# Performance work log

Measured on AMD Instinct MI355X. Metric: run time of the kernel, lower is better.

## Reference

```python
import jax, jax.numpy as jnp
import numpy as np

ALPHA = 1.0
MIN_FEATURE_SIZE = 1.0
SC = 1e-12                      # stabilizer added to first derivatives
EPS_V_FLOOR = 1e-32 / 6.0       # torch.tensor(1e-32 ** 1 / 6) == 1e-32/6 (** binds tighter than /)


def _grad2d(phi, d):
    """Vectorized equivalent of numerical_gradient_2d: central differences in the
    interior, one-sided forward/backward differences at the boundaries."""
    gx = jnp.concatenate([
        (phi[1:2, :] - phi[0:1, :]) / d,           # forward diff at i == 0
        (phi[2:, :] - phi[:-2, :]) / (2.0 * d),    # central diff in interior
        (phi[-1:, :] - phi[-2:-1, :]) / d,         # backward diff at i == H-1
    ], axis=0)
    gy = jnp.concatenate([
        (phi[:, 1:2] - phi[:, 0:1]) / d,
        (phi[:, 2:] - phi[:, :-2]) / (2.0 * d),
        (phi[:, -1:] - phi[:, -2:-1]) / d,
    ], axis=1)
    return gx, gy


def setup_inputs() -> dict:
    key = jax.random.key(0)
    eps = jax.random.normal(key, (4096, 4096), dtype=jnp.float32)
    grid_size = jnp.asarray(0.05, dtype=jnp.float32)
    return {"eps": eps, "grid_size": grid_size}


def reference(eps, grid_size):
    # mirror the field along axis 1 (torch.cat((eps, eps.flip(1)), dim=1)) -> [H, 2W]
    eps = jnp.concatenate([eps, eps[:, ::-1]], axis=1)

    # ls_derivatives: first derivatives (+SC), then second derivatives of those
    eps_x, eps_y = _grad2d(eps, grid_size)
    eps_x = eps_x + SC
    eps_y = eps_y + SC
    eps_xx, eps_xy = _grad2d(eps_x, grid_size)
    _, eps_yy = _grad2d(eps_y, grid_size)

    pi_d = np.pi / (1.1 * MIN_FEATURE_SIZE)
    eps_v = jnp.maximum(jnp.sqrt(eps_x**2 + eps_y**2), EPS_V_FLOOR)
    k = (eps_x**2 * eps_yy - 2.0 * eps_x * eps_y * eps_xy + eps_y**2 * eps_xx) / eps_v**3
    curve_const = jnp.abs(k * jnp.arctan(eps_v / eps)) - pi_d
    return jnp.nansum(ALPHA * jnp.maximum(curve_const, 0.0) * grid_size**2)
```

## Files before the change

### kernel.cpp

```cpp
#include <hip/hip_runtime.h>
#include <math.h>


#define BLOCK_X 256
#define ROWS_PER 16

__device__ __forceinline__ float fast_atan_ratio(float v, float c, float rv)
{
    const float rc = __builtin_amdgcn_rcpf(c);
    const float q  = v * rc;
    const float iq = c * rv;
    const bool  big = fabsf(q) > 1.0f;
    const float t  = big ? iq : q;
    const float s  = t * t;
    float p = fmaf(s, -0.01172120f, 0.05265332f);
    p = fmaf(s, p, -0.11643287f);
    p = fmaf(s, p,  0.19354346f);
    p = fmaf(s, p, -0.33262347f);
    p = fmaf(s, p,  0.99997726f);
    const float at = p * t;
    const float hp = copysignf(1.57079632679f, q);
    return big ? (hp - at) : at;
}

__device__ __forceinline__ float interior_rows(
    const float* __restrict__ eps, int Wn, int i0, int j, float rd2)
{
    const float SC = 1e-12f;
    const float FLOORV = (float)(1e-32 / 6.0);
    const float pi_d = 3.14159265358979323846f / 1.1f;
    const float rd22 = rd2 * rd2;

    const float* p0 = eps + (size_t)(i0 - 2) * (size_t)Wn + j;
    const float* p1 = p0 + Wn;
    const float* p2 = p1 + Wn;
    const float* p3 = p2 + Wn;
    const float* p4 = p3 + Wn;

    float acc = 0.0f;
    #pragma unroll
    for (int r = 0; r < ROWS_PER; ++r) {
        const float e_nn = p0[0];
        const float e_nw = p1[-1], e_n = p1[0], e_ne = p1[1];
        const float e_ww = p2[-2], e_w = p2[-1], e_c = p2[0],
                    e_e  = p2[1],  e_ee = p2[2];
        const float e_sw = p3[-1], e_s = p3[0], e_se = p3[1];
        const float e_ss = p4[0];

        const float ex = fmaf(e_s - e_n, rd2, SC);
        const float ey = fmaf(e_e - e_w, rd2, SC);
        const float exx = fmaf(-2.0f, e_c, e_ss + e_nn) * rd22;
        const float eyy = fmaf(-2.0f, e_c, e_ee + e_ww) * rd22;
        const float exy = ((e_se - e_ne) - (e_sw - e_nw)) * rd22;

        const float t1 = ex * ex;
        const float t2 = ey * ey;
        const float exy2 = exy + exy;
        float num = t1 * eyy;
        num = fmaf(t2, exx, num);
        num = fmaf(-(ex * ey), exy2, num);

        float ev = __builtin_amdgcn_sqrtf(t1 + t2);
        ev = fmaxf(ev, FLOORV);
        const float rv = __builtin_amdgcn_rcpf(ev);
        const float k  = num * (rv * rv) * rv;
        const float at = fast_atan_ratio(ev, e_c, rv);
        const float cc = fabsf(k * at) - pi_d;
        acc += fmaxf(cc, 0.0f);

        p0 = p1; p1 = p2; p2 = p3; p3 = p4; p4 += Wn;
    }
    return acc;
}

__device__ float generic_rows(const float* __restrict__ eps, int Hn, int Wn,
                              int i0, int j, float rd)
{
    const float rd2 = 0.5f * rd;
    const float SC = 1e-12f;
    const float FLOORV = (float)(1e-32 / 6.0);
    const float pi_d = 3.14159265358979323846f / 1.1f;

    const int jm  = (j > 0) ? j - 1 : 0;
    const int jmm = (j > 1) ? j - 2 : 0;
    const int jp = j + 1, jpp = j + 2;
    const int cjp  = (jp  < Wn) ? jp  : (2 * Wn - 1 - jp);
    const int cjpp = (jpp < Wn) ? jpp : (2 * Wn - 1 - jpp);
    const float syj = (j == 0)  ? rd : rd2;
    const float sym = (jm == 0) ? rd : rd2;
    const float syp = rd2;

    float acc = 0.0f;
    for (int r = 0; r < ROWS_PER; ++r) {
        const int i = i0 + r;
        if (i >= Hn) break;
        const int im  = (i > 0) ? i - 1 : 0;
        const int ip  = (i < Hn - 1) ? i + 1 : Hn - 1;
        const int imm = (im > 0) ? im - 1 : 0;
        const int ipp = (ip < Hn - 1) ? ip + 1 : Hn - 1;
        const float sxi = (i == 0 || i == Hn - 1) ? rd : rd2;
        const float sxm = (im == 0) ? rd : rd2;
        const float sxp = (ip == Hn - 1) ? rd : rd2;

        const float* rowc  = eps + (size_t)i   * (size_t)Wn;
        const float* rown  = eps + (size_t)im  * (size_t)Wn;
        const float* rows_ = eps + (size_t)ip  * (size_t)Wn;
        const float* rownn = eps + (size_t)imm * (size_t)Wn;
        const float* rowss = eps + (size_t)ipp * (size_t)Wn;

        const float e_c  = rowc[j];
        const float e_n  = rown[j],   e_s  = rows_[j];
        const float e_nn = rownn[j],  e_ss = rowss[j];
        const float e_w  = rowc[jm],  e_e  = rowc[cjp];
        const float e_ww = rowc[jmm], e_ee = rowc[cjpp];
        const float e_nw = rown[jm],  e_ne = rown[cjp];
        const float e_sw = rows_[jm], e_se = rows_[cjp];

        const float ex = fmaf(e_s - e_n, sxi, SC);
        const float ey = fmaf(e_e - e_w, syj, SC);
        float exn = fmaf(e_c - e_nn, sxm, SC);
        float exs = fmaf(e_ss - e_c, sxp, SC);
        if (i == 0)      exn = ex;
        if (i == Hn - 1) exs = ex;
        const float exx = (exs - exn) * sxi;
        float eyw = fmaf(e_c - e_ww, sym, SC);
        const float eye = fmaf(e_ee - e_c, syp, SC);
        if (j == 0) eyw = ey;
        const float eyy = (eye - eyw) * syj;
        const float exy = ((e_se - e_ne) - (e_sw - e_nw)) * (sxi * syj);

        const float t1 = ex * ex;
        const float t2 = ey * ey;
        float num = t1 * eyy;
        num = fmaf(t2, exx, num);
        num = fmaf(-2.0f * (ex * ey), exy, num);

        float ev = __builtin_amdgcn_sqrtf(t1 + t2);
        ev = fmaxf(ev, FLOORV);
        const float rv = __builtin_amdgcn_rcpf(ev);
        const float k  = num * (rv * rv) * rv;
        const float at = fast_atan_ratio(ev, e_c, rv);
        const float cc = fabsf(k * at) - pi_d;
        acc += fmaxf(cc, 0.0f);
    }
    return acc;
}

__global__ __launch_bounds__(BLOCK_X, 4) void curve_partial_kernel(
    const float* __restrict__ eps, const float* __restrict__ gs,
    double* __restrict__ partial, int Hn, int Wn)
{
    const int tx = threadIdx.x;
    const int j  = blockIdx.x * BLOCK_X + tx;
    const int i0 = blockIdx.y * ROWS_PER;
    const float rd = 1.0f / gs[0];
    const float rd2 = 0.5f * rd;

    float accf;
    const bool row_int = (i0 >= 2) && (i0 + ROWS_PER + 1 < Hn);
    const bool col_int = (j >= 2) && (j + 2 < Wn);
    if (row_int && col_int)
        accf = interior_rows(eps, Wn, i0, j, rd2);
    else
        accf = generic_rows(eps, Hn, Wn, i0, j, rd);

    double acc = (double)accf;
    #pragma unroll
    for (int off = 32; off > 0; off >>= 1)
        acc += __shfl_down(acc, off, 64);
    __shared__ double lds[BLOCK_X / 64];
    const int lane = tx & 63, wv = tx >> 6;
    if (lane == 0) lds[wv] = acc;
    __syncthreads();
    if (tx == 0) {
        partial[blockIdx.y * gridDim.x + blockIdx.x] =
            lds[0] + lds[1] + lds[2] + lds[3];
    }
}

__global__ __launch_bounds__(256) void curve_finish_kernel(
    const double* __restrict__ partial, int n,
    const float* __restrict__ gs, float* __restrict__ out)
{
    const int tx = threadIdx.x;
    double acc = 0.0;
    for (int idx = tx; idx < n; idx += 256) acc += partial[idx];
    #pragma unroll
    for (int off = 32; off > 0; off >>= 1)
        acc += __shfl_down(acc, off, 64);
    __shared__ double lds[4];
    const int lane = tx & 63, wv = tx >> 6;
    if (lane == 0) lds[wv] = acc;
    __syncthreads();
    if (tx == 0) {
        const double d = (double)gs[0];
        out[0] = (float)((lds[0] + lds[1] + lds[2] + lds[3]) * 2.0 * d * d);
    }
}

extern "C" void kernel_launch(void* const* d_in, const int* in_sizes, int n_in,
                              void* d_out, int out_size, void* d_ws, size_t ws_size,
                              hipStream_t stream) {
    const float* eps = (const float*)d_in[0];
    const float* gs  = (const float*)d_in[1];
    float* out = (float*)d_out;

    const int n = in_sizes[0];
    int Wn = (int)(sqrt((double)n) + 0.5);
    int Hn = n / Wn;

    const int gx = (Wn + BLOCK_X - 1) / BLOCK_X;
    const int gy = (Hn + ROWS_PER - 1) / ROWS_PER;
    double* partial = (double*)d_ws;

    curve_partial_kernel<<<dim3(gx, gy), BLOCK_X, 0, stream>>>(eps, gs, partial, Hn, Wn);
    curve_finish_kernel<<<1, 256, 0, stream>>>(partial, gx * gy, gs, out);
}
```

Baseline: 121.8 us.

## Stage stencil tile with halo in LDS instead of redundant global loads

Measured after the change: 120.8 us. No clear change (-0.8%).

```diff
diff --git a/kernel.cpp b/kernel.cpp
--- a/kernel.cpp
+++ b/kernel.cpp
@@ -4,6 +4,8 @@
 
 #define BLOCK_X 256
 #define ROWS_PER 16
+#define TILE_W (BLOCK_X + 4)
+#define TILE_H (ROWS_PER + 4)
 
 __device__ __forceinline__ float fast_atan_ratio(float v, float c, float rv)
 {
@@ -23,29 +25,30 @@
     return big ? (hp - at) : at;
 }
 
-__device__ __forceinline__ float interior_rows(
-    const float* __restrict__ eps, int Wn, int i0, int j, float rd2)
+__device__ __forceinline__ float lds_rows(const float* __restrict__ tile,
+                                          int tx, float rd2)
 {
     const float SC = 1e-12f;
     const float FLOORV = (float)(1e-32 / 6.0);
     const float pi_d = 3.14159265358979323846f / 1.1f;
     const float rd22 = rd2 * rd2;
 
-    const float* p0 = eps + (size_t)(i0 - 2) * (size_t)Wn + j;
-    const float* p1 = p0 + Wn;
-    const float* p2 = p1 + Wn;
-    const float* p3 = p2 + Wn;
-    const float* p4 = p3 + Wn;
-
     float acc = 0.0f;
     #pragma unroll
     for (int r = 0; r < ROWS_PER; ++r) {
-        const float e_nn = p0[0];
-        const float e_nw = p1[-1], e_n = p1[0], e_ne = p1[1];
-        const float e_ww = p2[-2], e_w = p2[-1], e_c = p2[0],
-                    e_e  = p2[1],  e_ee = p2[2];
-        const float e_sw = p3[-1], e_s = p3[0], e_se = p3[1];
-        const float e_ss = p4[0];
+        const float e_nn = tile[(r + 0) * TILE_W + tx + 2];
+        const float e_nw = tile[(r + 1) * TILE_W + tx + 1];
+        const float e_n  = tile[(r + 1) * TILE_W + tx + 2];
+        const float e_ne = tile[(r + 1) * TILE_W + tx + 3];
+        const float e_ww = tile[(r + 2) * TILE_W + tx + 0];
+        const float e_w  = tile[(r + 2) * TILE_W + tx + 1];
+        const float e_c  = tile[(r + 2) * TILE_W + tx + 2];
+        const float e_e  = tile[(r + 2) * TILE_W + tx + 3];
+        const float e_ee = tile[(r + 2) * TILE_W + tx + 4];
+        const float e_sw = tile[(r + 3) * TILE_W + tx + 1];
+        const float e_s  = tile[(r + 3) * TILE_W + tx + 2];
+        const float e_se = tile[(r + 3) * TILE_W + tx + 3];
+        const float e_ss = tile[(r + 4) * TILE_W + tx + 2];
 
         const float ex = fmaf(e_s - e_n, rd2, SC);
         const float ey = fmaf(e_e - e_w, rd2, SC);
@@ -67,8 +70,6 @@
         const float at = fast_atan_ratio(ev, e_c, rv);
         const float cc = fabsf(k * at) - pi_d;
         acc += fmaxf(cc, 0.0f);
-
-        p0 = p1; p1 = p2; p2 = p3; p3 = p4; p4 += Wn;
     }
     return acc;
 }
@@ -146,35 +147,81 @@
     return acc;
 }
 
-__global__ __launch_bounds__(BLOCK_X, 4) void curve_partial_kernel(
+__global__ __launch_bounds__(BLOCK_X) void curve_partial_kernel(
     const float* __restrict__ eps, const float* __restrict__ gs,
     double* __restrict__ partial, int Hn, int Wn)
 {
+    __shared__ float tile[TILE_H * TILE_W];
     const int tx = threadIdx.x;
-    const int j  = blockIdx.x * BLOCK_X + tx;
+    const int jb = blockIdx.x * BLOCK_X;
+    const int j  = jb + tx;
     const int i0 = blockIdx.y * ROWS_PER;
     const float rd = 1.0f / gs[0];
     const float rd2 = 0.5f * rd;
 
-    float accf;
-    const bool row_int = (i0 >= 2) && (i0 + ROWS_PER + 1 < Hn);
-    const bool col_int = (j >= 2) && (j + 2 < Wn);
-    if (row_int && col_int)
-        accf = interior_rows(eps, Wn, i0, j, rd2);
-    else
-        accf = generic_rows(eps, Hn, Wn, i0, j, rd);
+    const bool row_int = (i0 >= 2) && (i0 + ROWS_PER + 2 <= Hn);
+
+    float accf = 0.0f;
+    if (row_int) {
+        const bool cint = (jb >= 2) && (jb + BLOCK_X + 2 <= Wn);
+        const float* g = eps + (size_t)(i0 - 2) * (size_t)Wn;
+        if (cint) {
+            const float* gm = g + (jb - 2) + tx;
+            float buf[TILE_H];
+            #pragma unroll
+            for (int r = 0; r < TILE_H; ++r) buf[r] = gm[(size_t)r * Wn];
+            #pragma unroll
+            for (int r = 0; r < TILE_H; ++r) tile[r * TILE_W + tx] = buf[r];
+            if (tx < 4) {
+                const float* gt = gm + BLOCK_X;
+                float bt[TILE_H];
+                #pragma unroll
+                for (int r = 0; r < TILE_H; ++r) bt[r] = gt[(size_t)r * Wn];
+                #pragma unroll
+                for (int r = 0; r < TILE_H; ++r)
+                    tile[r * TILE_W + BLOCK_X + tx] = bt[r];
+            }
+        } else {
+            int c0 = jb - 2 + tx;
+            c0 = (c0 < 0) ? 0 : ((c0 >= Wn) ? 2 * Wn - 1 - c0 : c0);
+            float buf[TILE_H];
+            #pragma unroll
+            for (int r = 0; r < TILE_H; ++r) buf[r] = g[(size_t)r * Wn + c0];
+            #pragma unroll
+            for (int r = 0; r < TILE_H; ++r) tile[r * TILE_W + tx] = buf[r];
+            if (tx < 4) {
+                int c1 = jb + 2 + BLOCK_X + tx - 4 + 2;
+                c1 = (c1 < 0) ? 0 : ((c1 >= Wn) ? 2 * Wn - 1 - c1 : c1);
+                float bt[TILE_H];
+                #pragma unroll
+                for (int r = 0; r < TILE_H; ++r) bt[r] = g[(size_t)r * Wn + c1];
+                #pragma unroll
+                for (int r = 0; r < TILE_H; ++r)
+                    tile[r * TILE_W + BLOCK_X + tx] = bt[r];
+            }
+        }
+        __syncthreads();
+
+        if (j >= 2 && j < Wn)
+            accf = lds_rows(tile, tx, rd2);
+        else if (j < Wn)
+            accf = generic_rows(eps, Hn, Wn, i0, j, rd);
+    } else {
+        if (j < Wn)
+            accf = generic_rows(eps, Hn, Wn, i0, j, rd);
+    }
 
     double acc = (double)accf;
     #pragma unroll
     for (int off = 32; off > 0; off >>= 1)
         acc += __shfl_down(acc, off, 64);
-    __shared__ double lds[BLOCK_X / 64];
+    __shared__ double ldsr[BLOCK_X / 64];
     const int lane = tx & 63, wv = tx >> 6;
-    if (lane == 0) lds[wv] = acc;
+    if (lane == 0) ldsr[wv] = acc;
     __syncthreads();
     if (tx == 0) {
         partial[blockIdx.y * gridDim.x + blockIdx.x] =
-            lds[0] + lds[1] + lds[2] + lds[3];
+            ldsr[0] + ldsr[1] + ldsr[2] + ldsr[3];
     }
 }
 
```
